# Optimization experiments

Measured on AMD Instinct MI355X. Metric: run time of the kernel, lower is better.

## Reference

```python
import jax, jax.numpy as jnp
import numpy as np

BS = 128          # batch size (baked into trans_bs = Linear(bs, 1))
SEQ = 100         # raw seq len; InnerComp concat doubles it to 200
D = 64            # user/item embedding dim
HID = 128         # predictor hidden dim
NITEM = 1000000   # item vocab
NNEG = 99         # negative samples (test mode)
TH1 = 0.007       # InnerComp threshold (~1/BS)
TH2 = 0.007       # InterComp threshold


def setup_inputs() -> dict:
    key = jax.random.key(0)
    ks = list(jax.random.split(key, 40))
    def nrm(i, shape, s=0.05):
        return jax.random.normal(ks[i], shape, jnp.float32) * s
    inp = {
        "u_node": jax.random.randint(ks[0], (BS,), 0, NITEM),
        "i_node": jax.random.randint(ks[1], (BS,), 0, NITEM),
        "neg_samples": jax.random.randint(ks[2], (BS, NNEG), 0, NITEM),
        "seq_d1": jax.random.randint(ks[3], (BS, SEQ), 0, NITEM),
        "seq_d2": jax.random.randint(ks[4], (BS, SEQ), 0, NITEM),
        "long_tail_mask_d1": jax.random.randint(ks[5], (BS, SEQ), 0, 2),
        "long_tail_mask_d2": jax.random.randint(ks[6], (BS, SEQ), 0, 2),
        "emb": nrm(7, (NITEM, D)),
    }
    j = 8
    for name in ["inc1", "inc2", "itc1", "itc2"]:
        inp[name + "_Wnn"] = nrm(j, (D, D)); j += 1
        inp[name + "_bnn"] = nrm(j, (D,)); j += 1
        inp[name + "_Wbs"] = nrm(j, (1, BS)); j += 1
        inp[name + "_bbs"] = nrm(j, (1,)); j += 1
    for name in ["gru1", "gru2"]:
        inp[name + "_Wih"] = nrm(j, (3 * D, D)); j += 1
        inp[name + "_Whh"] = nrm(j, (3 * D, D)); j += 1
        inp[name + "_bih"] = nrm(j, (3 * D,)); j += 1
        inp[name + "_bhh"] = nrm(j, (3 * D,)); j += 1
    inp["fc1_W"] = nrm(j, (HID, 2 * D)); j += 1
    inp["fc1_b"] = nrm(j, (HID,)); j += 1
    inp["fc2_W"] = nrm(j, (1, HID)); j += 1
    inp["fc2_b"] = nrm(j, (1,)); j += 1
    return inp


def _comp(seq_self, seq_other, Wnn, bnn, Wbs, bbs, th):
    # Faithful collapse of InnerComp/InterComp: in the torch code,
    # group_bool[i,j] = max(seq_self[j] @ seq_other[j]^T) is independent of i,
    # and so is the trans_bs output. Same math, no O(bs^2 L^2) blowup.
    g = jnp.max(jnp.einsum('bld,bmd->blm', seq_self, seq_other), axis=(1, 2))  # [bs]
    m = (jax.nn.softmax(g) > th).astype(seq_self.dtype)                        # [bs]
    y = (seq_other * m[:, None, None]) @ Wnn.T + bnn                           # [bs,L,d]
    z = jnp.einsum('j,jld->ld', Wbs[0], y) + bbs[0]                            # [L,d]
    z = jnp.broadcast_to(z[None], seq_self.shape)
    return jnp.concatenate([seq_self, z], axis=1)                              # [bs,2L,d]


def _gru(x, Wih, Whh, bih, bhh):
    # torch.nn.GRU, 1 layer, batch_first, h0 = 0. Gate order: r, z, n.
    B, L, _ = x.shape
    H = Whh.shape[1]
    xp = x @ Wih.T + bih  # [B,L,3H] precomputed input projections
    def step(h, xt):
        gh = h @ Whh.T + bhh
        xr, xz, xn = jnp.split(xt, 3, axis=-1)
        hr, hz, hn = jnp.split(gh, 3, axis=-1)
        r = jax.nn.sigmoid(xr + hr)
        z = jax.nn.sigmoid(xz + hz)
        n = jnp.tanh(xn + r * hn)
        hnew = (1 - z) * n + z * h
        return hnew, hnew
    h0 = jnp.zeros((B, H), x.dtype)
    _, hs = jax.lax.scan(step, h0, jnp.swapaxes(xp, 0, 1))
    return jnp.swapaxes(hs, 0, 1)  # [B,L,H]


def reference(u_node, i_node, neg_samples, seq_d1, seq_d2,
              long_tail_mask_d1, long_tail_mask_d2, emb,
              inc1_Wnn, inc1_bnn, inc1_Wbs, inc1_bbs,
              inc2_Wnn, inc2_bnn, inc2_Wbs, inc2_bbs,
              itc1_Wnn, itc1_bnn, itc1_Wbs, itc1_bbs,
              itc2_Wnn, itc2_bnn, itc2_Wbs, itc2_bbs,
              gru1_Wih, gru1_Whh, gru1_bih, gru1_bhh,
              gru2_Wih, gru2_Whh, gru2_bih, gru2_bhh,
              fc1_W, fc1_b, fc2_W, fc2_b):
    i_feat = emb[i_node][:, None, :]     # [bs,1,d]
    neg_feat = emb[neg_samples]          # [bs,99,d]
    s1 = emb[seq_d1]                     # [bs,SEQ,d]
    s2 = emb[seq_d2]
    # InnerComp (self-comparison), doubles seq len
    s1 = _comp(s1, s1, inc1_Wnn, inc1_bnn, inc1_Wbs, inc1_bbs, TH1)
    s2 = _comp(s2, s2, inc2_Wnn, inc2_bnn, inc2_Wbs, inc2_bbs, TH1)
    # GRU per domain
    s1 = _gru(s1, gru1_Wih, gru1_Whh, gru1_bih, gru1_bhh)
    s2 = _gru(s2, gru2_Wih, gru2_Whh, gru2_bih, gru2_bhh)
    # InterComp (cross-domain), doubles seq len again
    s1n = _comp(s1, s2, itc1_Wnn, itc1_bnn, itc1_Wbs, itc1_bbs, TH2)
    s2n = _comp(s2, s1, itc2_Wnn, itc2_bnn, itc2_Wbs, itc2_bbs, TH2)
    u1 = jnp.mean(s1n, axis=1)           # [bs,d]
    u2 = jnp.mean(s2n, axis=1)
    i_all = jnp.concatenate([i_feat, neg_feat], axis=1)  # [bs,100,d]
    def pred(u):
        c = jnp.concatenate([jnp.broadcast_to(u[:, None, :], i_all.shape), i_all], axis=-1)
        h = jax.nn.relu(c @ fc1_W.T + fc1_b)
        return jax.nn.sigmoid(h @ fc2_W.T + fc2_b)[..., 0]  # [bs,100]
    return pred(u1), pred(u2)
```

## Files before the change

### kernel.cpp

```cpp
#include <hip/hip_runtime.h>
#include <hip/hip_bf16.h>
#include <cstdint>
#include <cstddef>

#define TH 0.007f

#define OFF_S1RAW   0u
#define OFF_S2RAW   819200u
#define OFF_IALL    1638400u
#define OFF_GRU1O   2457600u
#define OFF_GRU2O   4096000u
#define OFF_XP1     5734400u
#define OFF_XP2     8192000u
#define OFF_ZP1     10649600u
#define OFF_ZP2     10668800u
#define OFF_ZINC1   10688000u
#define OFF_ZINC2   10694400u
#define OFF_ZITC1   10700800u
#define OFF_ZITC2   10713600u
#define OFF_G3      10726400u
#define OFF_W4      10726784u
#define OFF_C4      10727296u
#define OFF_U1      10727300u
#define OFF_U2      10735492u

__device__ __forceinline__ float sigf(float x) { return 1.0f / (1.0f + __expf(-x)); }
__device__ __forceinline__ float tanhf_(float x) { return 1.0f - 2.0f / (__expf(2.0f * x) + 1.0f); }
__device__ __forceinline__ float rl(float v, int l) {
  return __int_as_float(__builtin_amdgcn_readlane(__float_as_int(v), l));
}

__global__ void k_gather(const int* __restrict__ i_node, const int* __restrict__ neg,
                         const int* __restrict__ seq1, const int* __restrict__ seq2,
                         const float* __restrict__ emb, float* __restrict__ ws) {
  int tid = threadIdx.x;
  int r = blockIdx.x * 4 + (tid >> 6);
  int d = tid & 63;
  long idx;
  float* dst;
  if (r < 12800) {
    idx = seq1[r];
    dst = ws + OFF_S1RAW + (size_t)r * 64;
  } else if (r < 25600) {
    int rr = r - 12800;
    idx = seq2[rr];
    dst = ws + OFF_S2RAW + (size_t)rr * 64;
  } else {
    int rr = r - 25600;
    int b = rr / 100, i = rr % 100;
    idx = (i == 0) ? i_node[b] : neg[b * 99 + i - 1];
    dst = ws + OFF_IALL + (size_t)rr * 64;
  }
  dst[d] = emb[idx * 64 + d];
}

__global__ __launch_bounds__(256) void k_gmax(const float* __restrict__ A0, const float* __restrict__ B0, float* g0,
                                              const float* __restrict__ A1, const float* __restrict__ B1, float* g1,
                                              int L, int nbhalf) {
  int half = blockIdx.x / nbhalf;
  int b = blockIdx.x % nbhalf;
  const float* A = half ? A1 : A0;
  const float* B = half ? B1 : B0;
  float* gout = half ? g1 : g0;
  __shared__ __align__(16) float SA[64 * 104];
  __shared__ __align__(16) float SB[64 * 104];
  __shared__ float red[4];
  int tid = threadIdx.x;
  int nch = L / 100;
  float gm = -1e30f;
  for (int ai = 0; ai < nch; ++ai) {
    for (int bi = 0; bi < nch; ++bi) {
      __syncthreads();
      for (int e = tid; e < 6400; e += 256) {
        int l = e >> 6, k = e & 63;
        SA[k * 104 + l] = A[((size_t)b * L + ai * 100 + l) * 64 + k];
        SB[k * 104 + l] = B[((size_t)b * L + bi * 100 + l) * 64 + k];
      }
      __syncthreads();
      for (int id = tid; id < 625; id += 256) {
        int ti = id / 25, tj = id % 25;
        int l0 = ti * 4, m0 = tj * 4;
        float acc[4][4];
#pragma unroll
        for (int x = 0; x < 4; ++x)
#pragma unroll
          for (int y = 0; y < 4; ++y) acc[x][y] = 0.0f;
#pragma unroll 16
        for (int k = 0; k < 64; ++k) {
          const float4 av = *reinterpret_cast<const float4*>(&SA[k * 104 + l0]);
          const float4 bv = *reinterpret_cast<const float4*>(&SB[k * 104 + m0]);
          float aa[4] = {av.x, av.y, av.z, av.w};
          float bb[4] = {bv.x, bv.y, bv.z, bv.w};
#pragma unroll
          for (int x = 0; x < 4; ++x)
#pragma unroll
            for (int y = 0; y < 4; ++y) acc[x][y] = fmaf(aa[x], bb[y], acc[x][y]);
        }
        float tm = acc[0][0];
#pragma unroll
        for (int x = 0; x < 4; ++x)
#pragma unroll
          for (int y = 0; y < 4; ++y) tm = fmaxf(tm, acc[x][y]);
        gm = fmaxf(gm, tm);
      }
    }
  }
  for (int off = 32; off; off >>= 1) gm = fmaxf(gm, __shfl_xor(gm, off, 64));
  if ((tid & 63) == 0) red[tid >> 6] = gm;
  __syncthreads();
  if (tid == 0) gout[b] = fmaxf(fmaxf(red[0], red[1]), fmaxf(red[2], red[3]));
}

__global__ void k_mask(const float* g0, const float* Wbs0, float* w0, float* c0,
                       const float* g1, const float* Wbs1, float* w1, float* c1) {
  int blk = blockIdx.x, tid = threadIdx.x;
  const float* g = blk ? g1 : g0;
  const float* Wbs = blk ? Wbs1 : Wbs0;
  float* w = blk ? w1 : w0;
  float* c = blk ? c1 : c0;
  __shared__ float ra[2], rb[2], rc[2];
  float gv = g[tid];
  float mx = gv;
  for (int off = 32; off; off >>= 1) mx = fmaxf(mx, __shfl_xor(mx, off, 64));
  if ((tid & 63) == 0) ra[tid >> 6] = mx;
  __syncthreads();
  mx = fmaxf(ra[0], ra[1]);
  float e = __expf(gv - mx);
  float sm = e;
  for (int off = 32; off; off >>= 1) sm += __shfl_xor(sm, off, 64);
  if ((tid & 63) == 0) rb[tid >> 6] = sm;
  __syncthreads();
  float soft = e / (rb[0] + rb[1]);
  float wb = Wbs[tid];
  w[tid] = (soft > TH) ? wb : 0.0f;
  float cs = wb;
  for (int off = 32; off; off >>= 1) cs += __shfl_xor(cs, off, 64);
  if ((tid & 63) == 0) rc[tid >> 6] = cs;
  __syncthreads();
  if (tid == 0) c[0] = rc[0] + rc[1];
}

__global__ void k_z(const float* o0, const float* w0, const float* Wnn0, const float* bnn0, const float* c0, const float* bbs0, float* z0,
                    const float* o1, const float* w1, const float* Wnn1, const float* bnn1, const float* c1, const float* bbs1, float* z1,
                    int L) {
  int comp = blockIdx.x / L;
  int l = blockIdx.x % L;
  const float* other = comp ? o1 : o0;
  const float* wv = comp ? w1 : w0;
  const float* Wnn = comp ? Wnn1 : Wnn0;
  const float* bnn = comp ? bnn1 : bnn0;
  const float* cp = comp ? c1 : c0;
  const float* bbs = comp ? bbs1 : bbs0;
  float* zout = comp ? z1 : z0;
  int d = threadIdx.x;
  float td = 0.0f;
#pragma unroll 4
  for (int j = 0; j < 128; ++j) td = fmaf(wv[j], other[((size_t)j * L + l) * 64 + d], td);
  __shared__ float tl[64];
  tl[d] = td;
  __syncthreads();
  float acc = fmaf(cp[0], bnn[d], bbs[0]);
#pragma unroll 8
  for (int k = 0; k < 64; ++k) acc = fmaf(tl[k], Wnn[d * 64 + k], acc);
  zout[l * 64 + d] = acc;
}

__global__ __launch_bounds__(192) void k_xproj(const float* __restrict__ s1raw, const float* __restrict__ s2raw,
                                               const float* __restrict__ zi1, const float* __restrict__ zi2,
                                               const float* __restrict__ W1, const float* __restrict__ b1,
                                               const float* __restrict__ W2, const float* __restrict__ b2,
                                               float* xp1, float* xp2, float* zp1, float* zp2) {
  int blk = blockIdx.x;
  const float* X;
  const float* W;
  const float* bi;
  float* out;
  int nrows, lb;
  if (blk < 800)        { X = s1raw; W = W1; bi = b1; out = xp1; nrows = 12800; lb = blk; }
  else if (blk < 1600)  { X = s2raw; W = W2; bi = b2; out = xp2; nrows = 12800; lb = blk - 800; }
  else if (blk < 1607)  { X = zi1;   W = W1; bi = b1; out = zp1; nrows = 100;   lb = blk - 1600; }
  else                  { X = zi2;   W = W2; bi = b2; out = zp2; nrows = 100;   lb = blk - 1607; }
  int row0 = lb * 16;
  int j = threadIdx.x;
  __shared__ float xt[16 * 64];
  int rmax = nrows - row0;
  if (rmax > 16) rmax = 16;
  int lim = rmax * 64;
  for (int e = j; e < lim; e += 192) xt[e] = X[(size_t)row0 * 64 + e];
  __syncthreads();
  float wreg[64];
#pragma unroll
  for (int k = 0; k < 64; ++k) wreg[k] = W[j * 64 + k];
  float bj = bi[j];
  for (int r = 0; r < rmax; ++r) {
    float acc = bj;
#pragma unroll
    for (int k = 0; k < 64; ++k) acc = fmaf(xt[r * 64 + k], wreg[k], acc);
    out[(size_t)(row0 + r) * 192 + j] = acc;
  }
}

__global__ __launch_bounds__(64, 1) void k_scan(const float* __restrict__ xp1, const float* __restrict__ xp2,
                                                const float* __restrict__ zp1, const float* __restrict__ zp2,
                                                const float* __restrict__ Whh1, const float* __restrict__ bhh1,
                                                const float* __restrict__ Whh2, const float* __restrict__ bhh2,
                                                float* o1, float* o2) {
  int dom = blockIdx.x >> 7;
  int bb = blockIdx.x & 127;
  const float* xp = dom ? xp2 : xp1;
  const float* zp = dom ? zp2 : zp1;
  const float* Whh = dom ? Whh2 : Whh1;
  const float* bhh = dom ? bhh2 : bhh1;
  float* out = (dom ? o2 : o1) + (size_t)bb * 200 * 64;
  int i = threadIdx.x;
  float wr[64], wz[64], wn[64];
#pragma unroll
  for (int k = 0; k < 64; ++k) {
    wr[k] = Whh[i * 64 + k];
    wz[k] = Whh[(64 + i) * 64 + k];
    wn[k] = Whh[(128 + i) * 64 + k];
  }
  float br = bhh[i], bz = bhh[64 + i], bn = bhh[128 + i];
  float h = 0.0f;
  const float* p0 = xp + (size_t)bb * 100 * 192;
  float xr = p0[i], xz = p0[64 + i], xn = p0[128 + i];
  for (int t = 0; t < 200; ++t) {
    float nxr = 0.f, nxz = 0.f, nxn = 0.f;
    if (t < 199) {
      const float* pn = (t + 1 < 100) ? xp + ((size_t)bb * 100 + (t + 1)) * 192
                                      : zp + (size_t)(t + 1 - 100) * 192;
      nxr = pn[i];
      nxz = pn[64 + i];
      nxn = pn[128 + i];
    }
    float ar = br, az = bz, an = bn;
#pragma unroll
    for (int k = 0; k < 64; ++k) {
      float hk = rl(h, k);
      ar = fmaf(hk, wr[k], ar);
      az = fmaf(hk, wz[k], az);
      an = fmaf(hk, wn[k], an);
    }
    float r = sigf(xr + ar);
    float z = sigf(xz + az);
    float n = tanhf_(xn + r * an);
    h = n + z * (h - n);
    out[t * 64 + i] = h;
    xr = nxr; xz = nxz; xn = nxn;
  }
}

__global__ void k_mean(const float* g1o, const float* g2o,
                       const float* zi1, const float* zi2,
                       float* u1, float* u2) {
  int dom = blockIdx.x >> 7, bb = blockIdx.x & 127, d = threadIdx.x;
  const float* s = dom ? g2o : g1o;
  const float* z = dom ? zi2 : zi1;
  float* u = dom ? u2 : u1;
  float acc = 0.0f;
  const float* sp = s + (size_t)bb * 200 * 64 + d;
#pragma unroll 4
  for (int t = 0; t < 200; ++t) acc += sp[t * 64];
#pragma unroll 4
  for (int l = 0; l < 200; ++l) acc += z[l * 64 + d];
  u[bb * 64 + d] = acc * 0.0025f;
}

__global__ __launch_bounds__(512, 2) void k_pred(const float* __restrict__ u1, const float* __restrict__ u2,
                                                 const float* __restrict__ iall,
                                                 const float* __restrict__ W1, const float* __restrict__ b1v,
                                                 const float* __restrict__ w2v, const float* __restrict__ b2v,
                                                 float* __restrict__ outp) {
  int p = blockIdx.x >> 7, bb = blockIdx.x & 127;
  const float* u = p ? u2 : u1;
  int tid = threadIdx.x;
  int j = tid & 127, g = tid >> 7, lane = tid & 63;
  float wrow[128];
#pragma unroll
  for (int k = 0; k < 128; ++k) wrow[k] = W1[j * 128 + k];
  float b1j = b1v[j], w2j = w2v[j], b2 = b2v[0];
  float ucopy = u[bb * 64 + lane];
  __shared__ float red[8];
  float* ob = outp + (size_t)p * 12800 + bb * 100;
  for (int m = 0; m < 25; ++m) {
    int i = g + 4 * m;
    float vcopy = iall[((size_t)bb * 100 + i) * 64 + lane];
    float acc = b1j;
#pragma unroll
    for (int k = 0; k < 64; ++k) acc = fmaf(rl(ucopy, k), wrow[k], acc);
#pragma unroll
    for (int k = 0; k < 64; ++k) acc = fmaf(rl(vcopy, k), wrow[64 + k], acc);
    float hg = fmaxf(acc, 0.0f);
    float part = w2j * hg;
    for (int off = 32; off; off >>= 1) part += __shfl_xor(part, off, 64);
    if (lane == 0) red[tid >> 6] = part;
    __syncthreads();
    if ((tid & 127) == 0) {
      float sres = red[tid >> 6] + red[(tid >> 6) + 1] + b2;
      ob[i] = 1.0f / (1.0f + __expf(-sres));
    }
    __syncthreads();
  }
}

extern "C" void kernel_launch(void* const* d_in, const int* in_sizes, int n_in,
                              void* d_out, int out_size, void* d_ws, size_t ws_size,
                              hipStream_t stream) {
  const int* i_node = (const int*)d_in[1];
  const int* neg = (const int*)d_in[2];
  const int* seq1 = (const int*)d_in[3];
  const int* seq2 = (const int*)d_in[4];
  const float* emb = (const float*)d_in[7];
  const float* inc1_Wnn = (const float*)d_in[8];
  const float* inc1_bnn = (const float*)d_in[9];
  const float* inc1_Wbs = (const float*)d_in[10];
  const float* inc1_bbs = (const float*)d_in[11];
  const float* inc2_Wnn = (const float*)d_in[12];
  const float* inc2_bnn = (const float*)d_in[13];
  const float* inc2_Wbs = (const float*)d_in[14];
  const float* inc2_bbs = (const float*)d_in[15];
  const float* itc1_Wnn = (const float*)d_in[16];
  const float* itc1_bnn = (const float*)d_in[17];
  const float* itc1_Wbs = (const float*)d_in[18];
  const float* itc1_bbs = (const float*)d_in[19];
  const float* itc2_Wnn = (const float*)d_in[20];
  const float* itc2_bnn = (const float*)d_in[21];
  const float* itc2_Wbs = (const float*)d_in[22];
  const float* itc2_bbs = (const float*)d_in[23];
  const float* gru1_Wih = (const float*)d_in[24];
  const float* gru1_Whh = (const float*)d_in[25];
  const float* gru1_bih = (const float*)d_in[26];
  const float* gru1_bhh = (const float*)d_in[27];
  const float* gru2_Wih = (const float*)d_in[28];
  const float* gru2_Whh = (const float*)d_in[29];
  const float* gru2_bih = (const float*)d_in[30];
  const float* gru2_bhh = (const float*)d_in[31];
  const float* fc1_W = (const float*)d_in[32];
  const float* fc1_b = (const float*)d_in[33];
  const float* fc2_W = (const float*)d_in[34];
  const float* fc2_b = (const float*)d_in[35];

  float* ws = (float*)d_ws;
  float* out = (float*)d_out;
  float* s1raw = ws + OFF_S1RAW;
  float* s2raw = ws + OFF_S2RAW;
  float* iall = ws + OFF_IALL;
  float* gru1o = ws + OFF_GRU1O;
  float* gru2o = ws + OFF_GRU2O;
  float* xp1 = ws + OFF_XP1;
  float* xp2 = ws + OFF_XP2;
  float* zp1 = ws + OFF_ZP1;
  float* zp2 = ws + OFF_ZP2;
  float* zinc1 = ws + OFF_ZINC1;
  float* zinc2 = ws + OFF_ZINC2;
  float* zitc1 = ws + OFF_ZITC1;
  float* zitc2 = ws + OFF_ZITC2;
  float* g3 = ws + OFF_G3;
  float* w4 = ws + OFF_W4;
  float* c4 = ws + OFF_C4;
  float* u1 = ws + OFF_U1;
  float* u2 = ws + OFF_U2;

  k_gather<<<9600, 256, 0, stream>>>(i_node, neg, seq1, seq2, emb, ws);
  k_gmax<<<256, 256, 0, stream>>>(s1raw, s1raw, g3, s2raw, s2raw, g3 + 128, 100, 128);
  k_mask<<<2, 128, 0, stream>>>(g3, inc1_Wbs, w4, c4, g3 + 128, inc2_Wbs, w4 + 128, c4 + 1);
  k_z<<<200, 64, 0, stream>>>(s1raw, w4, inc1_Wnn, inc1_bnn, c4, inc1_bbs, zinc1,
                              s2raw, w4 + 128, inc2_Wnn, inc2_bnn, c4 + 1, inc2_bbs, zinc2, 100);
  k_xproj<<<1614, 192, 0, stream>>>(s1raw, s2raw, zinc1, zinc2,
                                    gru1_Wih, gru1_bih, gru2_Wih, gru2_bih,
                                    xp1, xp2, zp1, zp2);
  k_scan<<<256, 64, 0, stream>>>(xp1, xp2, zp1, zp2, gru1_Whh, gru1_bhh, gru2_Whh, gru2_bhh,
                                 gru1o, gru2o);
  k_gmax<<<128, 256, 0, stream>>>(gru1o, gru2o, g3 + 256, gru1o, gru2o, g3 + 256, 200, 128);
  k_mask<<<2, 128, 0, stream>>>(g3 + 256, itc1_Wbs, w4 + 256, c4 + 2,
                                g3 + 256, itc2_Wbs, w4 + 384, c4 + 3);
  k_z<<<400, 64, 0, stream>>>(gru2o, w4 + 256, itc1_Wnn, itc1_bnn, c4 + 2, itc1_bbs, zitc1,
                              gru1o, w4 + 384, itc2_Wnn, itc2_bnn, c4 + 3, itc2_bbs, zitc2, 200);
  k_mean<<<256, 64, 0, stream>>>(gru1o, gru2o, zitc1, zitc2, u1, u2);
  k_pred<<<256, 512, 0, stream>>>(u1, u2, iall, fc1_W, fc1_b, fc2_W, fc2_b, out);
}
```

Measured before the change: 725.8 us.

## Fuse mask into k_z, split GRU gates across waves, restructure predictor

Folds the softmax-threshold mask computation into k_z, which removes two tiny kernel launches. The GRU scan now uses 192 threads so each wave computes one gate with weights held in registers and h broadcast from LDS. This replaces the per-k readlane chains with float4 LDS reads, at the cost of two block barriers per timestep. The predictor precomputes the u-part of fc1 once per block and assigns one item per thread, rather than doing a cross-wave reduction for every item.

```diff
diff --git a/kernel.cpp b/kernel.cpp
--- a/kernel.cpp
+++ b/kernel.cpp
@@ -19,16 +19,11 @@
 #define OFF_ZITC1   10700800u
 #define OFF_ZITC2   10713600u
 #define OFF_G3      10726400u
-#define OFF_W4      10726784u
-#define OFF_C4      10727296u
 #define OFF_U1      10727300u
 #define OFF_U2      10735492u
 
 __device__ __forceinline__ float sigf(float x) { return 1.0f / (1.0f + __expf(-x)); }
 __device__ __forceinline__ float tanhf_(float x) { return 1.0f - 2.0f / (__expf(2.0f * x) + 1.0f); }
-__device__ __forceinline__ float rl(float v, int l) {
-  return __int_as_float(__builtin_amdgcn_readlane(__float_as_int(v), l));
-}
 
 __global__ void k_gather(const int* __restrict__ i_node, const int* __restrict__ neg,
                          const int* __restrict__ seq1, const int* __restrict__ seq2,
@@ -111,55 +106,39 @@
   if (tid == 0) gout[b] = fmaxf(fmaxf(red[0], red[1]), fmaxf(red[2], red[3]));
 }
 
-__global__ void k_mask(const float* g0, const float* Wbs0, float* w0, float* c0,
-                       const float* g1, const float* Wbs1, float* w1, float* c1) {
-  int blk = blockIdx.x, tid = threadIdx.x;
-  const float* g = blk ? g1 : g0;
-  const float* Wbs = blk ? Wbs1 : Wbs0;
-  float* w = blk ? w1 : w0;
-  float* c = blk ? c1 : c0;
-  __shared__ float ra[2], rb[2], rc[2];
-  float gv = g[tid];
-  float mx = gv;
-  for (int off = 32; off; off >>= 1) mx = fmaxf(mx, __shfl_xor(mx, off, 64));
-  if ((tid & 63) == 0) ra[tid >> 6] = mx;
-  __syncthreads();
-  mx = fmaxf(ra[0], ra[1]);
-  float e = __expf(gv - mx);
-  float sm = e;
-  for (int off = 32; off; off >>= 1) sm += __shfl_xor(sm, off, 64);
-  if ((tid & 63) == 0) rb[tid >> 6] = sm;
-  __syncthreads();
-  float soft = e / (rb[0] + rb[1]);
-  float wb = Wbs[tid];
-  w[tid] = (soft > TH) ? wb : 0.0f;
-  float cs = wb;
-  for (int off = 32; off; off >>= 1) cs += __shfl_xor(cs, off, 64);
-  if ((tid & 63) == 0) rc[tid >> 6] = cs;
-  __syncthreads();
-  if (tid == 0) c[0] = rc[0] + rc[1];
-}
-
-__global__ void k_z(const float* o0, const float* w0, const float* Wnn0, const float* bnn0, const float* c0, const float* bbs0, float* z0,
-                    const float* o1, const float* w1, const float* Wnn1, const float* bnn1, const float* c1, const float* bbs1, float* z1,
+__global__ void k_z(const float* o0, const float* g0, const float* Wbs0, const float* Wnn0, const float* bnn0, const float* bbs0, float* z0,
+                    const float* o1, const float* g1, const float* Wbs1, const float* Wnn1, const float* bnn1, const float* bbs1, float* z1,
                     int L) {
   int comp = blockIdx.x / L;
   int l = blockIdx.x % L;
   const float* other = comp ? o1 : o0;
-  const float* wv = comp ? w1 : w0;
+  const float* g = comp ? g1 : g0;
+  const float* Wbs = comp ? Wbs1 : Wbs0;
   const float* Wnn = comp ? Wnn1 : Wnn0;
   const float* bnn = comp ? bnn1 : bnn0;
-  const float* cp = comp ? c1 : c0;
   const float* bbs = comp ? bbs1 : bbs0;
   float* zout = comp ? z1 : z0;
   int d = threadIdx.x;
+  __shared__ float w_s[128];
+  __shared__ float tl[64];
+  float ga = g[d], gb = g[d + 64];
+  float mx = fmaxf(ga, gb);
+  for (int off = 32; off; off >>= 1) mx = fmaxf(mx, __shfl_xor(mx, off, 64));
+  float ea = __expf(ga - mx), eb = __expf(gb - mx);
+  float sm = ea + eb;
+  for (int off = 32; off; off >>= 1) sm += __shfl_xor(sm, off, 64);
+  float wa = Wbs[d], wb = Wbs[d + 64];
+  w_s[d] = (ea / sm > TH) ? wa : 0.0f;
+  w_s[d + 64] = (eb / sm > TH) ? wb : 0.0f;
+  float cs = wa + wb;
+  for (int off = 32; off; off >>= 1) cs += __shfl_xor(cs, off, 64);
+  __syncthreads();
   float td = 0.0f;
 #pragma unroll 4
-  for (int j = 0; j < 128; ++j) td = fmaf(wv[j], other[((size_t)j * L + l) * 64 + d], td);
-  __shared__ float tl[64];
+  for (int j = 0; j < 128; ++j) td = fmaf(w_s[j], other[((size_t)j * L + l) * 64 + d], td);
   tl[d] = td;
   __syncthreads();
-  float acc = fmaf(cp[0], bnn[d], bbs[0]);
+  float acc = fmaf(cs, bnn[d], bbs[0]);
 #pragma unroll 8
   for (int k = 0; k < 64; ++k) acc = fmaf(tl[k], Wnn[d * 64 + k], acc);
   zout[l * 64 + d] = acc;
@@ -200,11 +179,11 @@
   }
 }
 
-__global__ __launch_bounds__(64, 1) void k_scan(const float* __restrict__ xp1, const float* __restrict__ xp2,
-                                                const float* __restrict__ zp1, const float* __restrict__ zp2,
-                                                const float* __restrict__ Whh1, const float* __restrict__ bhh1,
-                                                const float* __restrict__ Whh2, const float* __restrict__ bhh2,
-                                                float* o1, float* o2) {
+__global__ __launch_bounds__(192) void k_scan(const float* __restrict__ xp1, const float* __restrict__ xp2,
+                                              const float* __restrict__ zp1, const float* __restrict__ zp2,
+                                              const float* __restrict__ Whh1, const float* __restrict__ bhh1,
+                                              const float* __restrict__ Whh2, const float* __restrict__ bhh2,
+                                              float* o1, float* o2) {
   int dom = blockIdx.x >> 7;
   int bb = blockIdx.x & 127;
   const float* xp = dom ? xp2 : xp1;
@@ -212,41 +191,53 @@
   const float* Whh = dom ? Whh2 : Whh1;
   const float* bhh = dom ? bhh2 : bhh1;
   float* out = (dom ? o2 : o1) + (size_t)bb * 200 * 64;
-  int i = threadIdx.x;
-  float wr[64], wz[64], wn[64];
-#pragma unroll
-  for (int k = 0; k < 64; ++k) {
-    wr[k] = Whh[i * 64 + k];
-    wz[k] = Whh[(64 + i) * 64 + k];
-    wn[k] = Whh[(128 + i) * 64 + k];
-  }
-  float br = bhh[i], bz = bhh[64 + i], bn = bhh[128 + i];
-  float h = 0.0f;
-  const float* p0 = xp + (size_t)bb * 100 * 192;
-  float xr = p0[i], xz = p0[64 + i], xn = p0[128 + i];
+  int tid = threadIdx.x;
+  int g = tid >> 6;
+  int i = tid & 63;
+  __shared__ __align__(16) float h_s[64];
+  __shared__ float r_s[64];
+  __shared__ float z_s[64];
+  float w[64];
+  const float* wrow = Whh + (size_t)(g * 64 + i) * 64;
+#pragma unroll
+  for (int k4 = 0; k4 < 16; ++k4) {
+    float4 wv = *reinterpret_cast<const float4*>(wrow + 4 * k4);
+    w[4 * k4 + 0] = wv.x; w[4 * k4 + 1] = wv.y; w[4 * k4 + 2] = wv.z; w[4 * k4 + 3] = wv.w;
+  }
+  float bg = bhh[g * 64 + i];
+  if (tid < 64) h_s[tid] = 0.0f;
+  float h_i = 0.0f;
+  float x_cur = xp[((size_t)bb * 100) * 192 + g * 64 + i];
+  __syncthreads();
   for (int t = 0; t < 200; ++t) {
-    float nxr = 0.f, nxz = 0.f, nxn = 0.f;
+    float x_nxt = 0.0f;
     if (t < 199) {
-      const float* pn = (t + 1 < 100) ? xp + ((size_t)bb * 100 + (t + 1)) * 192
-                                      : zp + (size_t)(t + 1 - 100) * 192;
-      nxr = pn[i];
-      nxz = pn[64 + i];
-      nxn = pn[128 + i];
-    }
-    float ar = br, az = bz, an = bn;
-#pragma unroll
-    for (int k = 0; k < 64; ++k) {
-      float hk = rl(h, k);
-      ar = fmaf(hk, wr[k], ar);
-      az = fmaf(hk, wz[k], az);
-      an = fmaf(hk, wn[k], an);
-    }
-    float r = sigf(xr + ar);
-    float z = sigf(xz + az);
-    float n = tanhf_(xn + r * an);
-    h = n + z * (h - n);
-    out[t * 64 + i] = h;
-    xr = nxr; xz = nxz; xn = nxn;
+      const float* pn = (t < 99) ? xp + ((size_t)bb * 100 + t + 1) * 192
+                                 : zp + (size_t)(t + 1 - 100) * 192;
+      x_nxt = pn[g * 64 + i];
+    }
+    float a0 = bg, a1 = 0.0f, a2 = 0.0f, a3 = 0.0f;
+#pragma unroll
+    for (int k4 = 0; k4 < 16; ++k4) {
+      float4 hv = *reinterpret_cast<const float4*>(&h_s[4 * k4]);
+      a0 = fmaf(hv.x, w[4 * k4 + 0], a0);
+      a1 = fmaf(hv.y, w[4 * k4 + 1], a1);
+      a2 = fmaf(hv.z, w[4 * k4 + 2], a2);
+      a3 = fmaf(hv.w, w[4 * k4 + 3], a3);
+    }
+    float a = (a0 + a1) + (a2 + a3);
+    if (g == 0)      r_s[i] = sigf(x_cur + a);
+    else if (g == 1) z_s[i] = sigf(x_cur + a);
+    __syncthreads();
+    if (g == 2) {
+      float r = r_s[i], z = z_s[i];
+      float n = tanhf_(x_cur + r * a);
+      h_i = n + z * (h_i - n);
+      h_s[i] = h_i;
+      out[t * 64 + i] = h_i;
+    }
+    __syncthreads();
+    x_cur = x_nxt;
   }
 }
 
@@ -266,40 +257,55 @@
   u[bb * 64 + d] = acc * 0.0025f;
 }
 
-__global__ __launch_bounds__(512, 2) void k_pred(const float* __restrict__ u1, const float* __restrict__ u2,
-                                                 const float* __restrict__ iall,
-                                                 const float* __restrict__ W1, const float* __restrict__ b1v,
-                                                 const float* __restrict__ w2v, const float* __restrict__ b2v,
-                                                 float* __restrict__ outp) {
+__global__ __launch_bounds__(256) void k_pred(const float* __restrict__ u1, const float* __restrict__ u2,
+                                              const float* __restrict__ iall,
+                                              const float* __restrict__ W1, const float* __restrict__ b1v,
+                                              const float* __restrict__ w2v, const float* __restrict__ b2v,
+                                              float* __restrict__ outp) {
   int p = blockIdx.x >> 7, bb = blockIdx.x & 127;
-  const float* u = p ? u2 : u1;
+  const float* u = (p ? u2 : u1) + bb * 64;
   int tid = threadIdx.x;
-  int j = tid & 127, g = tid >> 7, lane = tid & 63;
-  float wrow[128];
-#pragma unroll
-  for (int k = 0; k < 128; ++k) wrow[k] = W1[j * 128 + k];
-  float b1j = b1v[j], w2j = w2v[j], b2 = b2v[0];
-  float ucopy = u[bb * 64 + lane];
-  __shared__ float red[8];
-  float* ob = outp + (size_t)p * 12800 + bb * 100;
-  for (int m = 0; m < 25; ++m) {
-    int i = g + 4 * m;
-    float vcopy = iall[((size_t)bb * 100 + i) * 64 + lane];
-    float acc = b1j;
-#pragma unroll
-    for (int k = 0; k < 64; ++k) acc = fmaf(rl(ucopy, k), wrow[k], acc);
-#pragma unroll
-    for (int k = 0; k < 64; ++k) acc = fmaf(rl(vcopy, k), wrow[64 + k], acc);
-    float hg = fmaxf(acc, 0.0f);
-    float part = w2j * hg;
-    for (int off = 32; off; off >>= 1) part += __shfl_xor(part, off, 64);
-    if (lane == 0) red[tid >> 6] = part;
-    __syncthreads();
-    if ((tid & 127) == 0) {
-      float sres = red[tid >> 6] + red[(tid >> 6) + 1] + b2;
-      ob[i] = 1.0f / (1.0f + __expf(-sres));
-    }
-    __syncthreads();
+  int lane = tid & 63;
+  int jh = (tid >> 6) & 1;
+  int ih = tid >> 7;
+  int i = ih * 64 + lane;
+  bool act = i < 100;
+  __shared__ float aU[128];
+  __shared__ float part[2][100];
+  if (tid < 128) {
+    int j = tid;
+    float acc = b1v[j];
+#pragma unroll 8
+    for (int k = 0; k < 64; ++k) acc = fmaf(u[k], W1[j * 128 + k], acc);
+    aU[j] = acc;
+  }
+  float V[64];
+  const float* vp = iall + ((size_t)bb * 100 + (act ? i : 0)) * 64;
+#pragma unroll
+  for (int k4 = 0; k4 < 16; ++k4) {
+    float4 vv = *reinterpret_cast<const float4*>(vp + 4 * k4);
+    V[4 * k4 + 0] = vv.x; V[4 * k4 + 1] = vv.y; V[4 * k4 + 2] = vv.z; V[4 * k4 + 3] = vv.w;
+  }
+  __syncthreads();
+  float acc_o = 0.0f;
+  for (int j = jh * 64; j < jh * 64 + 64; ++j) {
+    const float* wrow = W1 + j * 128 + 64;
+    float d0 = aU[j], d1 = 0.0f, d2 = 0.0f, d3 = 0.0f;
+#pragma unroll
+    for (int k = 0; k < 16; ++k) {
+      d0 = fmaf(V[4 * k + 0], wrow[4 * k + 0], d0);
+      d1 = fmaf(V[4 * k + 1], wrow[4 * k + 1], d1);
+      d2 = fmaf(V[4 * k + 2], wrow[4 * k + 2], d2);
+      d3 = fmaf(V[4 * k + 3], wrow[4 * k + 3], d3);
+    }
+    float hrelu = fmaxf((d0 + d1) + (d2 + d3), 0.0f);
+    acc_o = fmaf(w2v[j], hrelu, acc_o);
+  }
+  if (act) part[jh][i] = acc_o;
+  __syncthreads();
+  if (act && jh == 0) {
+    float s = part[0][i] + part[1][i] + b2v[0];
+    outp[(size_t)p * 12800 + bb * 100 + i] = 1.0f / (1.0f + __expf(-s));
   }
 }
 
@@ -356,26 +362,21 @@
   float* zitc1 = ws + OFF_ZITC1;
   float* zitc2 = ws + OFF_ZITC2;
   float* g3 = ws + OFF_G3;
-  float* w4 = ws + OFF_W4;
-  float* c4 = ws + OFF_C4;
   float* u1 = ws + OFF_U1;
   float* u2 = ws + OFF_U2;
 
   k_gather<<<9600, 256, 0, stream>>>(i_node, neg, seq1, seq2, emb, ws);
   k_gmax<<<256, 256, 0, stream>>>(s1raw, s1raw, g3, s2raw, s2raw, g3 + 128, 100, 128);
-  k_mask<<<2, 128, 0, stream>>>(g3, inc1_Wbs, w4, c4, g3 + 128, inc2_Wbs, w4 + 128, c4 + 1);
-  k_z<<<200, 64, 0, stream>>>(s1raw, w4, inc1_Wnn, inc1_bnn, c4, inc1_bbs, zinc1,
-                              s2raw, w4 + 128, inc2_Wnn, inc2_bnn, c4 + 1, inc2_bbs, zinc2, 100);
+  k_z<<<200, 64, 0, stream>>>(s1raw, g3, inc1_Wbs, inc1_Wnn, inc1_bnn, inc1_bbs, zinc1,
+                              s2raw, g3 + 128, inc2_Wbs, inc2_Wnn, inc2_bnn, inc2_bbs, zinc2, 100);
   k_xproj<<<1614, 192, 0, stream>>>(s1raw, s2raw, zinc1, zinc2,
                                     gru1_Wih, gru1_bih, gru2_Wih, gru2_bih,
                                     xp1, xp2, zp1, zp2);
-  k_scan<<<256, 64, 0, stream>>>(xp1, xp2, zp1, zp2, gru1_Whh, gru1_bhh, gru2_Whh, gru2_bhh,
-                                 gru1o, gru2o);
+  k_scan<<<256, 192, 0, stream>>>(xp1, xp2, zp1, zp2, gru1_Whh, gru1_bhh, gru2_Whh, gru2_bhh,
+                                  gru1o, gru2o);
   k_gmax<<<128, 256, 0, stream>>>(gru1o, gru2o, g3 + 256, gru1o, gru2o, g3 + 256, 200, 128);
-  k_mask<<<2, 128, 0, stream>>>(g3 + 256, itc1_Wbs, w4 + 256, c4 + 2,
-                                g3 + 256, itc2_Wbs, w4 + 384, c4 + 3);
-  k_z<<<400, 64, 0, stream>>>(gru2o, w4 + 256, itc1_Wnn, itc1_bnn, c4 + 2, itc1_bbs, zitc1,
-                              gru1o, w4 + 384, itc2_Wnn, itc2_bnn, c4 + 3, itc2_bbs, zitc2, 200);
+  k_z<<<400, 64, 0, stream>>>(gru2o, g3 + 256, itc1_Wbs, itc1_Wnn, itc1_bnn, itc1_bbs, zitc1,
+                              gru1o, g3 + 256, itc2_Wbs, itc2_Wnn, itc2_bnn, itc2_bbs, zitc2, 200);
   k_mean<<<256, 64, 0, stream>>>(gru1o, gru2o, zitc1, zitc2, u1, u2);
-  k_pred<<<256, 512, 0, stream>>>(u1, u2, iall, fc1_W, fc1_b, fc2_W, fc2_b, out);
-}
+  k_pred<<<256, 256, 0, stream>>>(u1, u2, iall, fc1_W, fc1_b, fc2_W, fc2_b, out);
+}
```

Measured after the change: 698.0 us. -3.8%, faster.
